# Optimization experiments

Measured on AMD Instinct MI355X. Metric: run time of the kernel, lower is better.

Reference implementation:

```python
import jax, jax.numpy as jnp
import numpy as np

N = 100000      # num nodes
M = 25000       # num hyperedges
E = 600000      # num incidences (node, hyperedge) pairs
D_IN, D_HID, D_OUT = 128, 128, 128


def setup_inputs() -> dict:
    key = jax.random.key(0)
    ks = jax.random.split(key, 9)
    s_in = 1.0 / np.sqrt(D_IN)
    s_hid = 1.0 / np.sqrt(D_HID)
    return {
        "x": jax.random.normal(ks[0], (N, D_IN), dtype=jnp.float32),
        "W1": jax.random.normal(ks[1], (D_IN, D_HID), dtype=jnp.float32) * s_in,
        "b1": jnp.zeros((D_HID,), dtype=jnp.float32),
        "W2": jax.random.normal(ks[2], (D_HID, D_HID), dtype=jnp.float32) * s_hid,
        "b2": jnp.zeros((D_HID,), dtype=jnp.float32),
        "W3": jax.random.normal(ks[3], (D_HID, D_OUT), dtype=jnp.float32) * s_hid,
        "b3": jnp.zeros((D_OUT,), dtype=jnp.float32),
        "node_idx": jax.random.randint(ks[4], (E,), 0, N, dtype=jnp.int32),
        "hedge_idx": jax.random.randint(ks[5], (E,), 0, M, dtype=jnp.int32),
        "num_hyperedges": M,
    }


def _hypergraph_conv(x, W, b, node_idx, hedge_idx, num_hyperedges):
    """PyG HypergraphConv (use_attention=False, hyperedge_weight=1):
    out = D^-1 H B^-1 H^T (x @ W) + b
    """
    n = x.shape[0]
    x = x @ W                                   # [N, F_out]
    ones = jnp.ones(node_idx.shape[0], dtype=x.dtype)
    deg_n = jax.ops.segment_sum(ones, node_idx, num_segments=n)              # D
    deg_e = jax.ops.segment_sum(ones, hedge_idx, num_segments=num_hyperedges)  # B
    d_inv = jnp.where(deg_n > 0, 1.0 / deg_n, 0.0)
    b_inv = jnp.where(deg_e > 0, 1.0 / deg_e, 0.0)
    # node -> hyperedge: m_e = B^-1 sum_{i in e} x_i
    m = jax.ops.segment_sum(x[node_idx], hedge_idx, num_segments=num_hyperedges)
    m = m * b_inv[:, None]
    # hyperedge -> node: out_i = D^-1 sum_{e ni i} m_e
    out = jax.ops.segment_sum(m[hedge_idx], node_idx, num_segments=n)
    out = out * d_inv[:, None]
    return out + b


def reference(x, W1, b1, W2, b2, W3, b3, node_idx, hedge_idx, num_hyperedges):
    # dropout is identity in eval mode (training=False)
    x = jax.nn.elu(_hypergraph_conv(x, W1, b1, node_idx, hedge_idx, num_hyperedges))
    x = jax.nn.elu(_hypergraph_conv(x, W2, b2, node_idx, hedge_idx, num_hyperedges))
    x = jax.nn.elu(_hypergraph_conv(x, W3, b3, node_idx, hedge_idx, num_hyperedges))
    return x
```

## Files before the change

### kernel.cpp

```cpp
#include <hip/hip_runtime.h>

#define NN 100000
#define MM 25000
#define EE 600000
#define TT (MM + NN)

#define NB 782
#define CAP 2048
#define TILE_E 2048
#define GA ((EE + TILE_E - 1) / TILE_E)
#define CVT_B 1024
#define ND_BLOCKS 2048

typedef __attribute__((ext_vector_type(8))) short short8;
typedef __attribute__((ext_vector_type(4))) float floatx4;

__device__ __forceinline__ float bl(unsigned int u){ return __uint_as_float(u << 16); }
__device__ __forceinline__ float bh(unsigned int u){ return __uint_as_float(u & 0xffff0000u); }
__device__ __forceinline__ unsigned int packbf2(float a, float b){
    unsigned int ua = __float_as_uint(a), ub = __float_as_uint(b);
    ua = (ua + 0x7fffu + ((ua >> 16) & 1u)) >> 16;
    ub = (ub + 0x7fffu + ((ub >> 16) & 1u)) & 0xffff0000u;
    return ua | ub;
}
__device__ __forceinline__ unsigned short f2bf(float f){
    unsigned int u = __float_as_uint(f);
    return (unsigned short)((u + 0x7fffu + ((u >> 16) & 1u)) >> 16);
}
__device__ __forceinline__ void acc8(float* a, uint4 v){
    a[0] += bl(v.x); a[1] += bh(v.x);
    a[2] += bl(v.y); a[3] += bh(v.y);
    a[4] += bl(v.z); a[5] += bh(v.z);
    a[6] += bl(v.w); a[7] += bh(v.w);
}

__global__ __launch_bounds__(256) void k_fused(const float* __restrict__ x, unsigned int* __restrict__ xb,
                        const float* __restrict__ W1, const float* __restrict__ W2,
                        const float* __restrict__ W3, unsigned short* __restrict__ WT,
                        const int* __restrict__ nidx, const int* __restrict__ hidx,
                        int* __restrict__ gcur, unsigned int* __restrict__ items) {
    __shared__ int h[1024];
    __shared__ int st[1024];
    __shared__ int tmp[256];
    __shared__ unsigned int g[2 * TILE_E];
    __shared__ unsigned short bk[2 * TILE_E];
    int b = blockIdx.x;
    int t = threadIdx.x;
    if (b < GA) {
        int base = b * TILE_E;
        int ne = min(TILE_E, EE - base);
        for (int i = t; i < 1024; i += 256) h[i] = 0;
        __syncthreads();
        #pragma unroll
        for (int k = 0; k < TILE_E / 256; k++) {
            int e = base + k * 256 + t;
            if (e < EE) {
                atomicAdd(&h[hidx[e] >> 6], 1);
                atomicAdd(&h[391 + (nidx[e] >> 8)], 1);
            }
        }
        __syncthreads();
        int c4[4]; int ts = 0;
        #pragma unroll
        for (int j = 0; j < 4; j++) { c4[j] = h[4 * t + j]; ts += c4[j]; }
        tmp[t] = ts;
        __syncthreads();
        for (int o = 1; o < 256; o <<= 1) {
            int u = (t >= o) ? tmp[t - o] : 0;
            __syncthreads();
            tmp[t] += u;
            __syncthreads();
        }
        int run = tmp[t] - ts;
        #pragma unroll
        for (int j = 0; j < 4; j++) { st[4 * t + j] = run; run += c4[j]; }
        __syncthreads();
        for (int i = t; i < NB; i += 256) {
            int c = h[i], s = st[i];
            if (c) {
                int gb = i * CAP + atomicAdd(&gcur[i], c);
                st[i] = gb - s;
            }
            h[i] = s;
        }
        __syncthreads();
        #pragma unroll
        for (int k = 0; k < TILE_E / 256; k++) {
            int e = base + k * 256 + t;
            if (e < EE) {
                int hh = hidx[e], nn = nidx[e];
                int b1 = hh >> 6;
                int p1 = atomicAdd(&h[b1], 1);
                g[p1] = ((unsigned)(hh & 63) << 17) | (unsigned)nn;
                bk[p1] = (unsigned short)b1;
                int b2 = 391 + (nn >> 8);
                int p2 = atomicAdd(&h[b2], 1);
                g[p2] = ((unsigned)(nn & 255) << 15) | (unsigned)hh;
                bk[p2] = (unsigned short)b2;
            }
        }
        __syncthreads();
        int total = 2 * ne;
        for (int p = t; p < total; p += 256) {
            items[st[bk[p]] + p] = g[p];
        }
    } else if (b < GA + CVT_B) {
        const int F4 = NN * 32;
        for (int u = (b - GA) * 1024; u < F4; u += CVT_B * 1024) {
            float4 v0 = ((const float4*)x)[u + t];
            float4 v1 = ((const float4*)x)[u + 256 + t];
            float4 v2 = ((const float4*)x)[u + 512 + t];
            float4 v3 = ((const float4*)x)[u + 768 + t];
            uint2 o0, o1, o2, o3;
            o0.x = packbf2(v0.x, v0.y); o0.y = packbf2(v0.z, v0.w);
            o1.x = packbf2(v1.x, v1.y); o1.y = packbf2(v1.z, v1.w);
            o2.x = packbf2(v2.x, v2.y); o2.y = packbf2(v2.z, v2.w);
            o3.x = packbf2(v3.x, v3.y); o3.y = packbf2(v3.z, v3.w);
            ((uint2*)xb)[u + t] = o0;
            ((uint2*)xb)[u + 256 + t] = o1;
            ((uint2*)xb)[u + 512 + t] = o2;
            ((uint2*)xb)[u + 768 + t] = o3;
        }
    } else {
        int l = b - GA - CVT_B;
        const float* W = l == 0 ? W1 : (l == 1 ? W2 : W3);
        unsigned short* T = WT + l * 16384;
        for (int i = t; i < 16384; i += 256) {
            int k = i >> 7, c = i & 127;
            T[c * 128 + k] = f2bf(W[k * 128 + c]);
        }
    }
}

__global__ __launch_bounds__(256) void k_passB(unsigned int* __restrict__ items,
                                               const int* __restrict__ gcur,
                                               int2* __restrict__ ptr2, float* __restrict__ inv,
                                               int* __restrict__ chist) {
    __shared__ unsigned int led[CAP];
    __shared__ unsigned int grp[CAP];
    __shared__ int bins[256], cur[256], tmp[256];
    __shared__ int chs[32];
    int b = blockIdx.x, t = threadIdx.x;
    int base = b * CAP, cnt = gcur[b];
    bool he = b < 391;
    int nbins = he ? 64 : 256;
    int keybase = he ? b * 64 : MM + (b - 391) * 256;
    int shift = he ? 17 : 15;
    unsigned int mask = he ? 0x1FFFFu : 0x7FFFu;
    int keylim = he ? MM : TT;

    for (int i = t; i < cnt; i += 256) led[i] = items[base + i];
    bins[t] = 0;
    if (t < 32) chs[t] = 0;
    __syncthreads();
    for (int i = t; i < cnt; i += 256) atomicAdd(&bins[led[i] >> shift], 1);
    __syncthreads();
    int v = (t < nbins) ? bins[t] : 0;
    tmp[t] = v;
    __syncthreads();
    for (int o = 1; o < 256; o <<= 1) {
        int u = (t >= o) ? tmp[t - o] : 0;
        __syncthreads();
        tmp[t] += u;
        __syncthreads();
    }
    int excl = tmp[t] - v;
    if (t < nbins) {
        int g = keybase + t;
        if (g < keylim) {
            ptr2[g] = make_int2(base + excl, v);
            inv[g] = v ? 1.f / (float)v : 0.f;
            int cls = min((v + 7) >> 3, 15);
            atomicAdd(&chs[cls + (he ? 0 : 16)], 1);
        }
        cur[t] = excl;
    }
    __syncthreads();
    for (int i = t; i < cnt; i += 256) {
        unsigned int it = led[i];
        int p = atomicAdd(&cur[it >> shift], 1);
        grp[p] = it & mask;
    }
    __syncthreads();
    for (int i = t; i < cnt; i += 256) items[base + i] = grp[i];
    if (t < 32 && chs[t]) atomicAdd(&chist[t], chs[t]);
}

#define SCAT_BLOCKS 128
__global__ __launch_bounds__(256) void k_scatter(const int2* __restrict__ ptr2,
                                                 const int* __restrict__ chist, int* __restrict__ ccur,
                                                 int* __restrict__ perm) {
    __shared__ int off[32];
    __shared__ int lh[32];
    __shared__ int lcur[32];
    int t = threadIdx.x;
    if (t < 32) {
        int side = t >> 4, c = t & 15;
        int s = 0;
        for (int k = 0; k < c; k++) s += chist[side * 16 + k];
        off[t] = s;
        lh[t] = 0;
    }
    __syncthreads();
    const int chunk = (TT + SCAT_BLOCKS - 1) / SCAT_BLOCKS;
    int beg = blockIdx.x * chunk;
    int end = min(beg + chunk, TT);
    for (int g = beg + t; g < end; g += 256) {
        int v = ptr2[g].y;
        int cls = min((v + 7) >> 3, 15);
        atomicAdd(&lh[(g < MM ? 0 : 16) + cls], 1);
    }
    __syncthreads();
    if (t < 32) {
        int c = lh[t];
        lcur[t] = c ? (off[t] + atomicAdd(&ccur[t], c)) : 0;
    }
    __syncthreads();
    for (int g = beg + t; g < end; g += 256) {
        int v = ptr2[g].y;
        int cls = min((v + 7) >> 3, 15);
        bool he = g < MM;
        int slot = atomicAdd(&lcur[(he ? 0 : 16) + cls], 1);
        perm[(he ? 0 : MM) + slot] = he ? g : (g - MM);
    }
}

__device__ __forceinline__ void gather_row8(const unsigned int* __restrict__ X,
                                            const unsigned int* __restrict__ adj,
                                            int beg, int deg, int ql, float* a) {
    if (deg <= 0) return;
    int end = beg + deg;
    int n[8];
    #pragma unroll
    for (int i = 0; i < 8; i++) n[i] = (beg + i < end) ? (int)adj[beg + i] : -1;
    for (int j = beg; j < end; j += 8) {
        int jn = j + 8;
        int m[8];
        #pragma unroll
        for (int i = 0; i < 8; i++) m[i] = (jn + i < end) ? (int)adj[jn + i] : -1;
        uint4 v[8];
        #pragma unroll
        for (int i = 0; i < 8; i++) {
            v[i] = make_uint4(0u, 0u, 0u, 0u);
            if (n[i] >= 0) v[i] = *((const uint4*)(X + (unsigned)n[i] * 64u) + ql);
        }
        #pragma unroll
        for (int i = 0; i < 8; i++) acc8(a, v[i]);
        #pragma unroll
        for (int i = 0; i < 8; i++) n[i] = m[i];
    }
}

__global__ __launch_bounds__(256) void k_hegemm(const unsigned int* __restrict__ X,
        const int2* __restrict__ ptr2, const unsigned int* __restrict__ adj,
        const float* __restrict__ b_inv, const unsigned short* __restrict__ WT,
        const int* __restrict__ hperm, unsigned short* __restrict__ C) {
    __shared__ unsigned int tile[16 * 68];
    __shared__ int prow[16];
    int t = threadIdx.x;
    int qidx = t >> 4, ql = t & 15;
    int r0 = blockIdx.x * 16;
    int r = r0 + qidx;
    float a[8] = {0.f,0.f,0.f,0.f,0.f,0.f,0.f,0.f};
    float sc = 0.f;
    if (r < MM) {
        int rt = hperm[r];
        if (ql == 0) prow[qidx] = rt;
        int2 pe = ptr2[rt];
        gather_row8(X, adj, pe.x, pe.y, ql, a);
        sc = b_inv[rt];
    } else if (ql == 0) {
        prow[qidx] = -1;
    }
    uint4 o;
    o.x = packbf2(a[0] * sc, a[1] * sc);
    o.y = packbf2(a[2] * sc, a[3] * sc);
    o.z = packbf2(a[4] * sc, a[5] * sc);
    o.w = packbf2(a[6] * sc, a[7] * sc);
    *((uint4*)(tile + qidx * 68 + ql * 4)) = o;
    __syncthreads();

    int wv = t >> 6, lane = t & 63;
    int mm = lane & 15, quad = lane >> 4;
    floatx4 acc0 = (floatx4){0.f,0.f,0.f,0.f}, acc1 = acc0;
    int c0 = wv * 2;
    #pragma unroll
    for (int q = 0; q < 4; q++) {
        short8 af = *reinterpret_cast<const short8*>((const short*)(tile + mm * 68) + q * 32 + quad * 8);
        short8 b0 = *reinterpret_cast<const short8*>(WT + (c0 * 16 + mm) * 128 + q * 32 + quad * 8);
        short8 b1 = *reinterpret_cast<const short8*>(WT + ((c0 + 1) * 16 + mm) * 128 + q * 32 + quad * 8);
        acc0 = __builtin_amdgcn_mfma_f32_16x16x32_bf16(af, b0, acc0, 0, 0, 0);
        acc1 = __builtin_amdgcn_mfma_f32_16x16x32_bf16(af, b1, acc1, 0, 0, 0);
    }
    #pragma unroll
    for (int rg = 0; rg < 4; rg++) {
        int rr = prow[quad * 4 + rg];
        if (rr >= 0) {
            C[rr * 128 + c0 * 16 + mm]       = f2bf(acc0[rg]);
            C[rr * 128 + (c0 + 1) * 16 + mm] = f2bf(acc1[rg]);
        }
    }
}

template<bool F32OUT>
__global__ __launch_bounds__(256) void k_gather_nd(const unsigned int* __restrict__ X,
        const int2* __restrict__ ptr2, const unsigned int* __restrict__ adj,
        const float* __restrict__ d_inv, const float* __restrict__ bias,
        const int* __restrict__ nperm, void* __restrict__ out) {
    int lane = threadIdx.x & 63, quad = lane >> 4, ql = lane & 15;
    int wave0 = (blockIdx.x * 256 + threadIdx.x) >> 6;
    const int NWAVES = ND_BLOCKS * 4;
    const float4* b4 = (const float4*)bias;
    float4 bA = b4[ql * 2], bB = b4[ql * 2 + 1];
    for (int rq = wave0; rq < NN / 4; rq += NWAVES) {
        int r = rq * 4 + quad;
        int rt = nperm[r];
        int2 pe = ptr2[rt];
        float a[8] = {0.f,0.f,0.f,0.f,0.f,0.f,0.f,0.f};
        gather_row8(X, adj, pe.x, pe.y, ql, a);
        float sc = d_inv[rt];
        float f[8];
        f[0] = a[0] * sc + bA.x; f[1] = a[1] * sc + bA.y;
        f[2] = a[2] * sc + bA.z; f[3] = a[3] * sc + bA.w;
        f[4] = a[4] * sc + bB.x; f[5] = a[5] * sc + bB.y;
        f[6] = a[6] * sc + bB.z; f[7] = a[7] * sc + bB.w;
        #pragma unroll
        for (int i = 0; i < 8; i++) f[i] = f[i] > 0.f ? f[i] : __expf(f[i]) - 1.f;
        if (F32OUT) {
            float* o = (float*)out + (unsigned)rt * 128u;
            ((float4*)o)[ql * 2]     = make_float4(f[0], f[1], f[2], f[3]);
            ((float4*)o)[ql * 2 + 1] = make_float4(f[4], f[5], f[6], f[7]);
        } else {
            uint4 o4;
            o4.x = packbf2(f[0], f[1]); o4.y = packbf2(f[2], f[3]);
            o4.z = packbf2(f[4], f[5]); o4.w = packbf2(f[6], f[7]);
            ((uint4*)((unsigned int*)out + (unsigned)rt * 64u))[ql] = o4;
        }
    }
}

extern "C" void kernel_launch(void* const* d_in, const int* in_sizes, int n_in,
                              void* d_out, int out_size, void* d_ws, size_t ws_size,
                              hipStream_t stream) {
    const float* x  = (const float*)d_in[0];
    const float* W1 = (const float*)d_in[1];
    const float* b1 = (const float*)d_in[2];
    const float* W2 = (const float*)d_in[3];
    const float* b2 = (const float*)d_in[4];
    const float* W3 = (const float*)d_in[5];
    const float* b3 = (const float*)d_in[6];
    const int* nidx = (const int*)d_in[7];
    const int* hidx = (const int*)d_in[8];

    char* ws = (char*)d_ws;
    size_t o = 0;
    auto alloc = [&](size_t b) -> char* { char* p = ws + o; o = (o + b + 255) & ~(size_t)255; return p; };
    int2*  ptr2  = (int2*)alloc((size_t)TT * 8);
    float* invq  = (float*)alloc(TT * 4);
    int*   gcur  = (int*)alloc((NB + 64) * 4);
    unsigned int* items = (unsigned int*)alloc((size_t)NB * CAP * 4);
    unsigned short* WT   = (unsigned short*)alloc(3 * 128 * 128 * 2);
    unsigned short* mbuf = (unsigned short*)alloc((size_t)MM * 128 * 2);
    int* perm = (int*)alloc((size_t)TT * 4);
    int* chist = gcur + NB;
    int* ccur  = chist + 32;

    unsigned int* xb   = (unsigned int*)d_out;
    unsigned int* bufA = (unsigned int*)d_out;
    unsigned int* bufB = (unsigned int*)d_out + (size_t)NN * 64;

    hipMemsetAsync(gcur, 0, (NB + 64) * 4, stream);
    k_fused<<<GA + CVT_B + 3, 256, 0, stream>>>(x, xb, W1, W2, W3, WT, nidx, hidx, gcur, items);
    k_passB<<<NB, 256, 0, stream>>>(items, gcur, ptr2, invq, chist);
    k_scatter<<<SCAT_BLOCKS, 256, 0, stream>>>(ptr2, chist, ccur, perm);

    const float* b_inv = invq;
    const float* d_inv = invq + MM;
    const int2* nptr2 = ptr2 + MM;
    const int* hperm = perm;
    const int* nperm = perm + MM;
    const int grid_hg = (MM + 15) / 16;
    const unsigned int* adj = items;

    k_hegemm<<<grid_hg, 256, 0, stream>>>(xb, ptr2, adj, b_inv, WT, hperm, mbuf);
    k_gather_nd<false><<<ND_BLOCKS, 256, 0, stream>>>((const unsigned int*)mbuf, nptr2, adj, d_inv, b1, nperm, (void*)bufA);
    k_hegemm<<<grid_hg, 256, 0, stream>>>(bufA, ptr2, adj, b_inv, WT + 16384, hperm, mbuf);
    k_gather_nd<false><<<ND_BLOCKS, 256, 0, stream>>>((const unsigned int*)mbuf, nptr2, adj, d_inv, b2, nperm, (void*)bufB);
    k_hegemm<<<grid_hg, 256, 0, stream>>>(bufB, ptr2, adj, b_inv, WT + 32768, hperm, mbuf);
    k_gather_nd<true ><<<ND_BLOCKS, 256, 0, stream>>>((const unsigned int*)mbuf, nptr2, adj, d_inv, b3, nperm, d_out);
}
```

Baseline: 322.6 us.

## Replace global atomic bucket reservation with count-scan-scatter passes for deterministic order

Tile bucket offsets no longer come from global atomicAdd on per-bucket cursors during the fused bucketing kernel. A separate counting kernel writes per-tile bucket histograms, and a scan kernel computes per-tile base offsets and bucket totals. The fused kernel then reads precomputed bases. This removes contention on global atomics and makes the item order within each bucket deterministic, which may improve locality downstream. The cost is two extra launches, an extra pass over the index arrays, and small extra workspace traffic.

```diff
diff --git a/kernel.cpp b/kernel.cpp
--- a/kernel.cpp
+++ b/kernel.cpp
@@ -34,11 +34,52 @@
     a[6] += bl(v.w); a[7] += bh(v.w);
 }
 
+__global__ __launch_bounds__(256) void k_count(const int* __restrict__ nidx, const int* __restrict__ hidx,
+                                               int* __restrict__ bcnt) {
+    __shared__ int h[NB];
+    int b = blockIdx.x, t = threadIdx.x;
+    for (int i = t; i < NB; i += 256) h[i] = 0;
+    __syncthreads();
+    int base = b * TILE_E;
+    #pragma unroll
+    for (int k = 0; k < TILE_E / 256; k++) {
+        int e = base + k * 256 + t;
+        if (e < EE) {
+            atomicAdd(&h[hidx[e] >> 6], 1);
+            atomicAdd(&h[391 + (nidx[e] >> 8)], 1);
+        }
+    }
+    __syncthreads();
+    for (int i = t; i < NB; i += 256) bcnt[b * NB + i] = h[i];
+}
+
+__global__ __launch_bounds__(256) void k_scan(const int* __restrict__ bcnt,
+                                              int* __restrict__ bases, int* __restrict__ gcur) {
+    __shared__ int tmp[256];
+    int i = blockIdx.x, t = threadIdx.x;
+    int e0 = 2 * t, e1 = 2 * t + 1;
+    int c0 = (e0 < GA) ? bcnt[e0 * NB + i] : 0;
+    int c1 = (e1 < GA) ? bcnt[e1 * NB + i] : 0;
+    int s = c0 + c1;
+    tmp[t] = s;
+    __syncthreads();
+    for (int o = 1; o < 256; o <<= 1) {
+        int u = (t >= o) ? tmp[t - o] : 0;
+        __syncthreads();
+        tmp[t] += u;
+        __syncthreads();
+    }
+    int excl = tmp[t] - s;
+    if (e0 < GA) bases[i * GA + e0] = i * CAP + excl;
+    if (e1 < GA) bases[i * GA + e1] = i * CAP + excl + c0;
+    if (t == 255) gcur[i] = tmp[255];
+}
+
 __global__ __launch_bounds__(256) void k_fused(const float* __restrict__ x, unsigned int* __restrict__ xb,
                         const float* __restrict__ W1, const float* __restrict__ W2,
                         const float* __restrict__ W3, unsigned short* __restrict__ WT,
                         const int* __restrict__ nidx, const int* __restrict__ hidx,
-                        int* __restrict__ gcur, unsigned int* __restrict__ items) {
+                        const int* __restrict__ bases, unsigned int* __restrict__ items) {
     __shared__ int h[1024];
     __shared__ int st[1024];
     __shared__ int tmp[256];
@@ -76,11 +117,8 @@
         for (int j = 0; j < 4; j++) { st[4 * t + j] = run; run += c4[j]; }
         __syncthreads();
         for (int i = t; i < NB; i += 256) {
-            int c = h[i], s = st[i];
-            if (c) {
-                int gb = i * CAP + atomicAdd(&gcur[i], c);
-                st[i] = gb - s;
-            }
+            int s = st[i];
+            if (h[i]) st[i] = bases[i * GA + b] - s;
             h[i] = s;
         }
         __syncthreads();
@@ -361,7 +399,9 @@
     unsigned int* items = (unsigned int*)alloc((size_t)NB * CAP * 4);
     unsigned short* WT   = (unsigned short*)alloc(3 * 128 * 128 * 2);
     unsigned short* mbuf = (unsigned short*)alloc((size_t)MM * 128 * 2);
-    int* perm = (int*)alloc((size_t)TT * 4);
+    int* perm  = (int*)alloc((size_t)TT * 4);
+    int* bcnt  = (int*)alloc((size_t)GA * NB * 4);
+    int* bases = (int*)alloc((size_t)NB * GA * 4);
     int* chist = gcur + NB;
     int* ccur  = chist + 32;
 
@@ -369,8 +409,10 @@
     unsigned int* bufA = (unsigned int*)d_out;
     unsigned int* bufB = (unsigned int*)d_out + (size_t)NN * 64;
 
-    hipMemsetAsync(gcur, 0, (NB + 64) * 4, stream);
-    k_fused<<<GA + CVT_B + 3, 256, 0, stream>>>(x, xb, W1, W2, W3, WT, nidx, hidx, gcur, items);
+    hipMemsetAsync(chist, 0, 64 * 4, stream);
+    k_count<<<GA, 256, 0, stream>>>(nidx, hidx, bcnt);
+    k_scan<<<NB, 256, 0, stream>>>(bcnt, bases, gcur);
+    k_fused<<<GA + CVT_B + 3, 256, 0, stream>>>(x, xb, W1, W2, W3, WT, nidx, hidx, bases, items);
     k_passB<<<NB, 256, 0, stream>>>(items, gcur, ptr2, invq, chist);
     k_scatter<<<SCAT_BLOCKS, 256, 0, stream>>>(ptr2, chist, ccur, perm);
 
```

Result: slower. 345.5 us (+7.1%).
